# Optimization experiments

Hardware: AMD Instinct MI355X
Metric: run time of the kernel (lower is better)

## Reference

```python
import jax, jax.numpy as jnp
import numpy as np

B, S, E, H = 2, 2048, 512, 8
D = E // H  # head size = 64
LN_EPS = 1e-5


def setup_inputs() -> dict:
    key = jax.random.key(0)
    ks = jax.random.split(key, 8)
    s_in = 1.0 / np.sqrt(E)
    return {
        "x": jax.random.normal(ks[0], (B, S, E), jnp.float32),
        # per-head projection weights, stored [H, E, D] so q = x @ Wq[h]
        "Wq": jax.random.normal(ks[1], (H, E, D), jnp.float32) * s_in,
        "Wk": jax.random.normal(ks[2], (H, E, D), jnp.float32) * s_in,
        "Wv": jax.random.normal(ks[3], (H, E, D), jnp.float32) * s_in,
        "Wp": jax.random.normal(ks[4], (E, E), jnp.float32) * s_in,
        "bp": jnp.zeros((E,), jnp.float32),
        "gamma": jnp.ones((E,), jnp.float32),
        "beta": jnp.zeros((E,), jnp.float32),
        # causal mask buffer: masked_fill where mask == 0
        "mask": jnp.tril(jnp.ones((S, S), jnp.int32)),
    }


def reference(x, Wq, Wk, Wv, Wp, bp, gamma, beta, mask):
    # batched per-head projections (equivalent to the H small Linears)
    q = jnp.einsum("bse,hed->bhsd", x, Wq)
    k = jnp.einsum("bse,hed->bhsd", x, Wk)
    v = jnp.einsum("bse,hed->bhsd", x, Wv)
    # NOTE: original has NO 1/sqrt(d) scaling
    att_log = jnp.einsum("bhsd,bhtd->bhst", q, k)
    att_log = jnp.where(mask == 0, -jnp.inf, att_log)
    att = jax.nn.softmax(att_log, axis=-1)
    o = jnp.einsum("bhst,bhtd->bhsd", att, v)  # [B,H,S,D]
    # torch.cat((val, values)) prepends each head -> final order head H-1 .. 0
    o = o[:, ::-1]
    vals = o.transpose(0, 2, 1, 3).reshape(B, S, E)
    out = vals @ Wp.T + bp + x
    mu = jnp.mean(out, axis=-1, keepdims=True)
    var = jnp.var(out, axis=-1, keepdims=True)
    return (out - mu) * jax.lax.rsqrt(var + LN_EPS) * gamma + beta
```

## Files before the change

kernel.cpp:

```cpp
#include <hip/hip_runtime.h>

constexpr int Bn = 2;
constexpr int Sn = 2048;
constexpr int En = 512;
constexpr int Hn = 8;
constexpr int Dn = 64;
constexpr int Mn = Bn * Sn;

typedef short bf8 __attribute__((ext_vector_type(8)));
typedef float f32x4 __attribute__((ext_vector_type(4)));

constexpr size_t XY = (size_t)Mn * En;
constexpr size_t WT = (size_t)3 * En * En;
constexpr size_t WP = (size_t)En * En;
constexpr size_t PL = (size_t)Bn * Hn * Sn * Dn;
constexpr size_t MLP = (size_t)512 * 64 * 2;
constexpr size_t OPP = (size_t)512 * 64 * 64;

__device__ __forceinline__ unsigned short f2bf(float f) {
    unsigned int u = __float_as_uint(f);
    unsigned int r = 0x7FFFu + ((u >> 16) & 1u);
    return (unsigned short)((u + r) >> 16);
}
__device__ __forceinline__ float bf2f(unsigned short u) {
    return __uint_as_float(((unsigned int)u) << 16);
}
__device__ __forceinline__ void split2(float f, unsigned short& hi, unsigned short& lo) {
    hi = f2bf(f);
    lo = f2bf(f - bf2f(hi));
}

__device__ __forceinline__ void g2l16(const unsigned short* g, unsigned short* l) {
    typedef __attribute__((address_space(1))) const unsigned int gu32;
    typedef __attribute__((address_space(3))) unsigned int lu32;
    __builtin_amdgcn_global_load_lds((gu32*)(unsigned long long)g,
                                     (lu32*)(unsigned int)(unsigned long long)l,
                                     16, 0, 0);
}

__global__ __launch_bounds__(256)
void prep(const float* __restrict__ x, const float* __restrict__ Wp,
          const float* __restrict__ Wq, const float* __restrict__ Wk,
          const float* __restrict__ Wv,
          unsigned short* __restrict__ xh, unsigned short* __restrict__ xl,
          unsigned short* __restrict__ Wph, unsigned short* __restrict__ Wpl,
          unsigned short* __restrict__ Wth, unsigned short* __restrict__ Wtl)
{
    __shared__ float t[64][65];
    const int bid = blockIdx.x;
    const int tid = threadIdx.x;

    if (bid < 1152) {
        const float* src = (bid < 1024) ? x : Wp;
        unsigned short* hp = (bid < 1024) ? xh : Wph;
        unsigned short* lp = (bid < 1024) ? xl : Wpl;
        const int blk = (bid < 1024) ? bid : (bid - 1024);
        const size_t base = ((size_t)blk * 256 + tid) * 8;
        float a[8];
        *(float4*)&a[0] = *(const float4*)(src + base);
        *(float4*)&a[4] = *(const float4*)(src + base + 4);
        unsigned short h[8], l[8];
        #pragma unroll
        for (int j = 0; j < 8; ++j) split2(a[j], h[j], l[j]);
        *(bf8*)(hp + base) = *(bf8*)&h[0];
        *(bf8*)(lp + base) = *(bf8*)&l[0];
        return;
    }

    const int idx = bid - 1152;
    const int ph = idx >> 3;
    const int proj = ph >> 3, h = ph & 7;
    const int e0 = (idx & 7) * 64;
    const float* W = (proj == 0) ? Wq : (proj == 1) ? Wk : Wv;
    const float* src = W + (size_t)h * En * Dn + (size_t)e0 * Dn;

    const int er = tid >> 2, cg = (tid & 3) * 16;
    #pragma unroll
    for (int c = 0; c < 4; ++c) {
        float4 v = *(const float4*)(src + (size_t)er * Dn + cg + 4 * c);
        t[er][cg + 4 * c + 0] = v.x;
        t[er][cg + 4 * c + 1] = v.y;
        t[er][cg + 4 * c + 2] = v.z;
        t[er][cg + 4 * c + 3] = v.w;
    }
    __syncthreads();

    const int d = tid >> 2, jg = (tid & 3) * 16;
    unsigned short h16[16], l16[16];
    #pragma unroll
    for (int j = 0; j < 16; ++j) split2(t[jg + j][d], h16[j], l16[j]);
    const size_t n = (size_t)proj * 512 + h * 64 + d;
    unsigned short* dh = Wth + n * En + e0 + jg;
    unsigned short* dl = Wtl + n * En + e0 + jg;
    *(bf8*)dh       = *(bf8*)&h16[0];
    *(bf8*)(dh + 8) = *(bf8*)&h16[8];
    *(bf8*)dl       = *(bf8*)&l16[0];
    *(bf8*)(dl + 8) = *(bf8*)&l16[8];
}

__global__ __launch_bounds__(256)
void qkv_gemm(const unsigned short* __restrict__ xh,
              const unsigned short* __restrict__ xl,
              const unsigned short* __restrict__ Wth,
              const unsigned short* __restrict__ Wtl,
              unsigned short* __restrict__ qh_g,
              unsigned short* __restrict__ ql_g,
              unsigned short* __restrict__ kh_g,
              unsigned short* __restrict__ kl_g,
              unsigned short* __restrict__ vT_g)
{
    __shared__ __align__(16) unsigned char smraw[49152];
    unsigned short* ldsAh = (unsigned short*)smraw;
    unsigned short* ldsAl = ldsAh + 8192;
    unsigned short* ldsBh = ldsAl + 8192;
    unsigned short* ldsBl = ldsBh + 4096;
    float (*Cf)[68] = (float(*)[68])(smraw);

    const int tid = threadIdx.x;
    const int m0 = blockIdx.x * 128;
    const int ny = blockIdx.y;
    const int proj = ny >> 3, h = ny & 7;

    const int wave = tid >> 6, lane = tid & 63;
    const int wm = (wave >> 1) * 64, wn = (wave & 1) * 32;
    const int lm = lane & 15, quad = lane >> 4;

    const int l4r = lane >> 2;
    const int l4c = (lane & 3) * 8;
    const unsigned short* gAh0 = xh + (size_t)(m0 + wave * 32 + l4r) * En + l4c;
    const unsigned short* gAh1 = gAh0 + (size_t)16 * En;
    const unsigned short* gAl0 = xl + (size_t)(m0 + wave * 32 + l4r) * En + l4c;
    const unsigned short* gAl1 = gAl0 + (size_t)16 * En;
    const unsigned short* gBh  = Wth + (size_t)(ny * 64 + wave * 16 + l4r) * En + l4c;
    const unsigned short* gBl  = Wtl + (size_t)(ny * 64 + wave * 16 + l4r) * En + l4c;
    const int offA = wave * 1024;
    const int offB = wave * 512;

    f32x4 acc[4][2];
    #pragma unroll
    for (int i = 0; i < 4; ++i)
        #pragma unroll
        for (int j = 0; j < 2; ++j) acc[i][j] = (f32x4){0.f, 0.f, 0.f, 0.f};

    g2l16(gAh0, ldsAh + offA);
    g2l16(gAh1, ldsAh + offA + 512);
    g2l16(gAl0, ldsAl + offA);
    g2l16(gAl1, ldsAl + offA + 512);
    g2l16(gBh,  ldsBh + offB);
    g2l16(gBl,  ldsBl + offB);

    int cur = 0;
    for (int k0 = 0; k0 < En; k0 += 32) {
        __syncthreads();
        const int nxt = cur ^ 1;
        if (k0 + 32 < En) {
            g2l16(gAh0 + k0 + 32, ldsAh + nxt * 4096 + offA);
            g2l16(gAh1 + k0 + 32, ldsAh + nxt * 4096 + offA + 512);
            g2l16(gAl0 + k0 + 32, ldsAl + nxt * 4096 + offA);
            g2l16(gAl1 + k0 + 32, ldsAl + nxt * 4096 + offA + 512);
            g2l16(gBh + k0 + 32,  ldsBh + nxt * 2048 + offB);
            g2l16(gBl + k0 + 32,  ldsBl + nxt * 2048 + offB);
        }

        const unsigned short* bAh = ldsAh + cur * 4096;
        const unsigned short* bAl = ldsAl + cur * 4096;
        const unsigned short* bBh = ldsBh + cur * 2048;
        const unsigned short* bBl = ldsBl + cur * 2048;
        bf8 a_h[4], a_l[4], b_h[2], b_l[2];
        #pragma unroll
        for (int mi = 0; mi < 4; ++mi) {
            a_h[mi] = *(const bf8*)(bAh + (wm + mi * 16 + lm) * 32 + quad * 8);
            a_l[mi] = *(const bf8*)(bAl + (wm + mi * 16 + lm) * 32 + quad * 8);
        }
        #pragma unroll
        for (int ni = 0; ni < 2; ++ni) {
            b_h[ni] = *(const bf8*)(bBh + (wn + ni * 16 + lm) * 32 + quad * 8);
            b_l[ni] = *(const bf8*)(bBl + (wn + ni * 16 + lm) * 32 + quad * 8);
        }
        #pragma unroll
        for (int mi = 0; mi < 4; ++mi)
            #pragma unroll
            for (int ni = 0; ni < 2; ++ni) {
                acc[mi][ni] = __builtin_amdgcn_mfma_f32_16x16x32_bf16(a_h[mi], b_h[ni], acc[mi][ni], 0, 0, 0);
                acc[mi][ni] = __builtin_amdgcn_mfma_f32_16x16x32_bf16(a_h[mi], b_l[ni], acc[mi][ni], 0, 0, 0);
                acc[mi][ni] = __builtin_amdgcn_mfma_f32_16x16x32_bf16(a_l[mi], b_h[ni], acc[mi][ni], 0, 0, 0);
            }
        cur = nxt;
    }
    __syncthreads();

    if (proj < 2) {
        unsigned short* hp = (proj == 0) ? qh_g : kh_g;
        unsigned short* lp = (proj == 0) ? ql_g : kl_g;
        #pragma unroll
        for (int p = 0; p < 2; ++p) {
            if ((wave >> 1) == p) {
                #pragma unroll
                for (int mi = 0; mi < 4; ++mi)
                    #pragma unroll
                    for (int ni = 0; ni < 2; ++ni)
                        #pragma unroll
                        for (int r = 0; r < 4; ++r)
                            Cf[mi * 16 + quad * 4 + r][wn + ni * 16 + lm] = acc[mi][ni][r];
            }
            __syncthreads();
            {
                const int lr = tid & 63;
                const int cg = (tid >> 6) * 16;
                const int m = m0 + p * 64 + lr;
                const int b = m >> 11, s = m & 2047;
                unsigned short hi[16], lo[16];
                #pragma unroll
                for (int j4 = 0; j4 < 4; ++j4) {
                    float4 v = *(const float4*)&Cf[lr][cg + 4 * j4];
                    split2(v.x, hi[4 * j4 + 0], lo[4 * j4 + 0]);
                    split2(v.y, hi[4 * j4 + 1], lo[4 * j4 + 1]);
                    split2(v.z, hi[4 * j4 + 2], lo[4 * j4 + 2]);
                    split2(v.w, hi[4 * j4 + 3], lo[4 * j4 + 3]);
                }
                const size_t base = (((size_t)(b * Hn + h) * Sn + s) * Dn) + cg;
                *(bf8*)(hp + base)     = *(bf8*)&hi[0];
                *(bf8*)(hp + base + 8) = *(bf8*)&hi[8];
                *(bf8*)(lp + base)     = *(bf8*)&lo[0];
                *(bf8*)(lp + base + 8) = *(bf8*)&lo[8];
            }
            __syncthreads();
        }
    } else {
        #pragma unroll
        for (int mi = 0; mi < 4; ++mi) {
            const int s0 = m0 + wm + mi * 16 + quad * 4;
            const int b = s0 >> 11, s = s0 & 2047;
            #pragma unroll
            for (int ni = 0; ni < 2; ++ni) {
                const int d = wn + ni * 16 + lm;
                ushort4 pk;
                pk.x = f2bf(acc[mi][ni][0]);
                pk.y = f2bf(acc[mi][ni][1]);
                pk.z = f2bf(acc[mi][ni][2]);
                pk.w = f2bf(acc[mi][ni][3]);
                *(ushort4*)(vT_g + ((size_t)(b * Hn + h) * Dn + d) * Sn + s) = pk;
            }
        }
    }
}

__global__ __launch_bounds__(512, 4)
void attn(const unsigned short* __restrict__ qh_g,
          const unsigned short* __restrict__ ql_g,
          const unsigned short* __restrict__ kh_g,
          const unsigned short* __restrict__ kl_g,
          const unsigned short* __restrict__ vT_g,
          unsigned short* __restrict__ Op,
          float* __restrict__ ml)
{
    extern __shared__ unsigned short sm[];
    unsigned short (*khs)[72] = (unsigned short(*)[72])(sm);
    unsigned short (*kls)[72] = (unsigned short(*)[72])(sm + 4608);
    unsigned short (*vTs)[72] = (unsigned short(*)[72])(sm + 9216);
    unsigned short (*pts)[72] = (unsigned short(*)[72])(sm + 13824);
    float* alf = (float*)(sm + 23040);

    const int bidx = blockIdx.x;
    const int xcd = bidx & 7;
    const int g = bidx >> 3;
    const int bh = xcd * 2 + (g & 1);
    const int p2 = g >> 1;
    const int qp = p2 & 15;
    const int sb = p2 >> 4;

    const int tid = threadIdx.x;
    const int wave = tid >> 6, lane = tid & 63;
    const int quad = lane >> 4, lq = lane & 15;
    const int wq = wave >> 2;
    const int w4 = wave & 3;

    const unsigned short* khb = kh_g + (size_t)bh * Sn * Dn;
    const unsigned short* klb = kl_g + (size_t)bh * Sn * Dn;
    const unsigned short* vTb = vT_g + (size_t)bh * Dn * Sn;

    const int srow = tid & 63;
    const int sdg  = tid >> 6;

    #pragma unroll 1
    for (int ph = 0; ph < 2; ++ph) {
        const int qt = ph ? (15 - qp) : qp;
        const int j  = ph ? (3 - sb) : sb;
        const int n  = 2 * qt + 2;
        const int its = (j * n) >> 2;
        const int ite = ((j + 1) * n) >> 2;
        const int qt64 = 2 * qt + wq;
        const int pslot = j * 512 + bh * 32 + qt64;
        const int dt = qt64;

        bf8 qfh[2], qfl[2];
        {
            const size_t qoff = ((size_t)bh * Sn + (size_t)qt * 128 + wave * 16 + lq) * Dn;
            #pragma unroll
            for (int c = 0; c < 2; ++c) {
                qfh[c] = *(const bf8*)(qh_g + qoff + c * 32 + quad * 8);
                qfl[c] = *(const bf8*)(ql_g + qoff + c * 32 + quad * 8);
            }
        }

        f32x4 accO[4];
        #pragma unroll
        for (int nj = 0; nj < 4; ++nj) accO[nj] = (f32x4){0.f, 0.f, 0.f, 0.f};
        float m = -1e30f, l = 0.f;

        bf8 pk0 = {0, 0, 0, 0, 0, 0, 0, 0};
        bf8 pl0 = {0, 0, 0, 0, 0, 0, 0, 0};
        bf8 pv0 = {0, 0, 0, 0, 0, 0, 0, 0};
        if (its < ite) {
            const int t0 = its * 64;
            pk0 = *(const bf8*)(khb + (size_t)(t0 + srow) * Dn + sdg * 8);
            pl0 = *(const bf8*)(klb + (size_t)(t0 + srow) * Dn + sdg * 8);
            pv0 = *(const bf8*)(vTb + (size_t)srow * Sn + t0 + sdg * 8);
        }

        for (int it = its; it < ite; ++it) {
            __syncthreads();
            *(bf8*)&khs[srow][sdg * 8] = pk0;
            *(bf8*)&kls[srow][sdg * 8] = pl0;
            *(bf8*)&vTs[srow][sdg * 8] = pv0;
            __syncthreads();

            if (it + 1 < ite) {
                const int t1 = (it + 1) * 64;
                pk0 = *(const bf8*)(khb + (size_t)(t1 + srow) * Dn + sdg * 8);
                pl0 = *(const bf8*)(klb + (size_t)(t1 + srow) * Dn + sdg * 8);
                pv0 = *(const bf8*)(vTb + (size_t)srow * Sn + t1 + sdg * 8);
            }

            if (it > dt) continue;

            f32x4 accS[4];
            #pragma unroll
            for (int mi = 0; mi < 4; ++mi) accS[mi] = (f32x4){0.f, 0.f, 0.f, 0.f};
            __builtin_amdgcn_s_setprio(1);
            #pragma unroll
            for (int mi = 0; mi < 4; ++mi) {
                #pragma unroll
                for (int c = 0; c < 2; ++c) {
                    bf8 ah = *(const bf8*)&khs[mi * 16 + lq][c * 32 + quad * 8];
                    bf8 al = *(const bf8*)&kls[mi * 16 + lq][c * 32 + quad * 8];
                    accS[mi] = __builtin_amdgcn_mfma_f32_16x16x32_bf16(ah, qfh[c], accS[mi], 0, 0, 0);
                    accS[mi] = __builtin_amdgcn_mfma_f32_16x16x32_bf16(ah, qfl[c], accS[mi], 0, 0, 0);
                    accS[mi] = __builtin_amdgcn_mfma_f32_16x16x32_bf16(al, qfh[c], accS[mi], 0, 0, 0);
                }
            }
            __builtin_amdgcn_s_setprio(0);

            if (it == dt) {
                const int qrel = w4 * 16 + lq;
                #pragma unroll
                for (int mi = 0; mi < 4; ++mi)
                    #pragma unroll
                    for (int r = 0; r < 4; ++r)
                        if (mi * 16 + quad * 4 + r > qrel) accS[mi][r] = -INFINITY;
            }

            float mt;
            {
                float t0 = fmaxf(fmaxf(accS[0][0], accS[0][1]), fmaxf(accS[0][2], accS[0][3]));
                float t1 = fmaxf(fmaxf(accS[1][0], accS[1][1]), fmaxf(accS[1][2], accS[1][3]));
                float t2 = fmaxf(fmaxf(accS[2][0], accS[2][1]), fmaxf(accS[2][2], accS[2][3]));
                float t3 = fmaxf(fmaxf(accS[3][0], accS[3][1]), fmaxf(accS[3][2], accS[3][3]));
                mt = fmaxf(fmaxf(t0, t1), fmaxf(t2, t3));
            }
            mt = fmaxf(mt, __shfl_xor(mt, 16));
            mt = fmaxf(mt, __shfl_xor(mt, 32));

            const bool defer = __all(mt <= m + 12.f);
            float mref, alpha = 1.f;
            if (defer) {
                mref = m;
            } else {
                mref = fmaxf(m, mt);
                alpha = __expf(m - mref);
            }

            float ls = 0.f;
            #pragma unroll
            for (int mi = 0; mi < 4; ++mi)
                #pragma unroll
                for (int r = 0; r < 4; ++r) {
                    const float p = __expf(accS[mi][r] - mref);
                    accS[mi][r] = p;
                    ls += p;
                }
            ls += __shfl_xor(ls, 16);
            ls += __shfl_xor(ls, 32);
            if (defer) {
                l += ls;
            } else {
                l = l * alpha + ls;
                m = mref;
            }

            #pragma unroll
            for (int mi = 0; mi < 4; ++mi) {
                ushort4 pk;
                pk.x = f2bf(accS[mi][0]);
                pk.y = f2bf(accS[mi][1]);
                pk.z = f2bf(accS[mi][2]);
                pk.w = f2bf(accS[mi][3]);
                *(ushort4*)&pts[wave * 16 + lq][mi * 16 + quad * 4] = pk;
            }

            if (!defer) {
                if (quad == 0) alf[wave * 16 + lq] = alpha;
                float4 al4 = *(const float4*)&alf[wave * 16 + quad * 4];
                #pragma unroll
                for (int nj = 0; nj < 4; ++nj) {
                    accO[nj][0] *= al4.x;
                    accO[nj][1] *= al4.y;
                    accO[nj][2] *= al4.z;
                    accO[nj][3] *= al4.w;
                }
            }

            __builtin_amdgcn_s_setprio(1);
            #pragma unroll
            for (int c = 0; c < 2; ++c) {
                bf8 pf = *(const bf8*)&pts[wave * 16 + lq][c * 32 + quad * 8];
                #pragma unroll
                for (int nj = 0; nj < 4; ++nj) {
                    bf8 vf = *(const bf8*)&vTs[nj * 16 + lq][c * 32 + quad * 8];
                    accO[nj] = __builtin_amdgcn_mfma_f32_16x16x32_bf16(pf, vf, accO[nj], 0, 0, 0);
                }
            }
            __builtin_amdgcn_s_setprio(0);
        }

        if (quad == 0) {
            const size_t mi_ = ((size_t)pslot * 64 + w4 * 16 + lq) * 2;
            ml[mi_]     = m;
            ml[mi_ + 1] = l;
        }
        #pragma unroll
        for (int r = 0; r < 4; ++r) {
            const int q = w4 * 16 + quad * 4 + r;
            unsigned short* dst = Op + ((size_t)pslot * 64 + q) * 64;
            #pragma unroll
            for (int nj = 0; nj < 4; ++nj)
                dst[nj * 16 + lq] = f2bf(accO[nj][r]);
        }
    }
}

__global__ __launch_bounds__(256)
void out_gemm(const unsigned short* __restrict__ Op,
              const float* __restrict__ ml,
              const unsigned short* __restrict__ Wph,
              const unsigned short* __restrict__ Wpl,
              const float* __restrict__ bp,
              const float* __restrict__ x,
              float* __restrict__ outp,
              float* __restrict__ outp2)
{
    __shared__ unsigned short Ah[64][40], Al[64][40];
    __shared__ __align__(16) unsigned short Bh[128][32], Bl[128][32];

    const int tid = threadIdx.x;
    const int m0 = blockIdx.x * 64;
    const int n0 = blockIdx.y * 128;
    const int kz = blockIdx.z;
    const int kbeg = kz * 256, kend = kbeg + 256;

    const int wave = tid >> 6, lane = tid & 63;
    const int wm = (wave >> 1) * 32, wn = (wave & 1) * 64;
    const int lm = lane & 15, quad = lane >> 4;

    const int am = tid >> 2;
    const int aks = (tid & 3) * 8;
    const int m_row = m0 + am;
    const int b_row = m_row >> 11, s_row = m_row & 2047;
    const int qt = s_row >> 6, qq = s_row & 63;

    float c0[4], c1[4], c2[4], c3[4];
    #pragma unroll
    for (int hl = 0; hl < 4; ++hl) {
        const int h = hl + (kz ? 0 : 4);
        const size_t base0 = (((size_t)(b_row * 8 + h) * 32 + qt) * 64 + qq) * 2;
        float mi_[4], li_[4];
        #pragma unroll
        for (int i = 0; i < 4; ++i) {
            mi_[i] = ml[base0 + i * MLP];
            li_[i] = ml[base0 + i * MLP + 1];
        }
        const float mn = fmaxf(fmaxf(mi_[0], mi_[1]), fmaxf(mi_[2], mi_[3]));
        const float a0 = __expf(mi_[0] - mn), a1 = __expf(mi_[1] - mn);
        const float a2 = __expf(mi_[2] - mn), a3 = __expf(mi_[3] - mn);
        const float inv = 1.f / (a0 * li_[0] + a1 * li_[1] + a2 * li_[2] + a3 * li_[3]);
        c0[hl] = a0 * inv;
        c1[hl] = a1 * inv;
        c2[hl] = a2 * inv;
        c3[hl] = a3 * inv;
    }

    const int l4r = lane >> 2;
    const int l4c = (lane & 3) * 8;
    const unsigned short* gB0h = Wph + (size_t)(n0 + wave * 32 + l4r) * En + l4c;
    const unsigned short* gB1h = gB0h + (size_t)16 * En;
    const unsigned short* gB0l = Wpl + (size_t)(n0 + wave * 32 + l4r) * En + l4c;
    const unsigned short* gB1l = gB0l + (size_t)16 * En;
    unsigned short* dB0h = &Bh[0][0] + wave * 1024;
    unsigned short* dB1h = dB0h + 512;
    unsigned short* dB0l = &Bl[0][0] + wave * 1024;
    unsigned short* dB1l = dB0l + 512;

    f32x4 acc[2][4];
    #pragma unroll
    for (int i = 0; i < 2; ++i)
        #pragma unroll
        for (int j = 0; j < 4; ++j) acc[i][j] = (f32x4){0.f, 0.f, 0.f, 0.f};

    bf8 po0, po1, po2, po3;
    {
        const int e0 = kbeg + aks;
        const int hh = 7 - (e0 >> 6);
        const int dd = e0 & 63;
        const size_t p0 = (((size_t)((b_row * 8 + hh) * 32 + qt)) * 64 + qq) * 64 + dd;
        po0 = *(const bf8*)(Op + p0);
        po1 = *(const bf8*)(Op + p0 + OPP);
        po2 = *(const bf8*)(Op + p0 + 2 * OPP);
        po3 = *(const bf8*)(Op + p0 + 3 * OPP);
    }

    for (int k0 = kbeg; k0 < kend; k0 += 32) {
        g2l16(gB0h + k0, dB0h);
        g2l16(gB1h + k0, dB1h);
        g2l16(gB0l + k0, dB0l);
        g2l16(gB1l + k0, dB1l);
        {
            const int hidx = (7 - ((k0 + aks) >> 6)) & 3;
            const float w0 = c0[hidx], w1 = c1[hidx];
            const float w2 = c2[hidx], w3 = c3[hidx];
            unsigned short hi[8], lo[8];
            #pragma unroll
            for (int j = 0; j < 8; ++j) {
                const float v = w0 * bf2f((unsigned short)po0[j]) +
                                w1 * bf2f((unsigned short)po1[j]) +
                                w2 * bf2f((unsigned short)po2[j]) +
                                w3 * bf2f((unsigned short)po3[j]);
                split2(v, hi[j], lo[j]);
            }
            *(bf8*)&Ah[am][aks] = *(bf8*)&hi[0];
            *(bf8*)&Al[am][aks] = *(bf8*)&lo[0];
        }
        __syncthreads();

        if (k0 + 32 < kend) {
            const int e0 = k0 + 32 + aks;
            const int hh = 7 - (e0 >> 6);
            const int dd = e0 & 63;
            const size_t p0 = (((size_t)((b_row * 8 + hh) * 32 + qt)) * 64 + qq) * 64 + dd;
            po0 = *(const bf8*)(Op + p0);
            po1 = *(const bf8*)(Op + p0 + OPP);
            po2 = *(const bf8*)(Op + p0 + 2 * OPP);
            po3 = *(const bf8*)(Op + p0 + 3 * OPP);
        }

        bf8 a_h[2], a_l[2], b_h[4], b_l[4];
        #pragma unroll
        for (int mi = 0; mi < 2; ++mi) {
            a_h[mi] = *(const bf8*)&Ah[wm + mi * 16 + lm][quad * 8];
            a_l[mi] = *(const bf8*)&Al[wm + mi * 16 + lm][quad * 8];
        }
        #pragma unroll
        for (int ni = 0; ni < 4; ++ni) {
            b_h[ni] = *(const bf8*)&Bh[wn + ni * 16 + lm][quad * 8];
            b_l[ni] = *(const bf8*)&Bl[wn + ni * 16 + lm][quad * 8];
        }
        #pragma unroll
        for (int mi = 0; mi < 2; ++mi)
            #pragma unroll
            for (int ni = 0; ni < 4; ++ni) {
                acc[mi][ni] = __builtin_amdgcn_mfma_f32_16x16x32_bf16(a_h[mi], b_h[ni], acc[mi][ni], 0, 0, 0);
                acc[mi][ni] = __builtin_amdgcn_mfma_f32_16x16x32_bf16(a_h[mi], b_l[ni], acc[mi][ni], 0, 0, 0);
                acc[mi][ni] = __builtin_amdgcn_mfma_f32_16x16x32_bf16(a_l[mi], b_h[ni], acc[mi][ni], 0, 0, 0);
            }
        __syncthreads();
    }

    float* dst = kz ? outp2 : outp;
    #pragma unroll
    for (int mi = 0; mi < 2; ++mi) {
        #pragma unroll
        for (int r = 0; r < 4; ++r) {
            const int m = m0 + wm + mi * 16 + quad * 4 + r;
            #pragma unroll
            for (int ni = 0; ni < 4; ++ni) {
                const int n = n0 + wn + ni * 16 + lm;
                const size_t idx = (size_t)m * En + n;
                const float extra = kz ? 0.f : (bp[n] + x[idx]);
                dst[idx] = acc[mi][ni][r] + extra;
            }
        }
    }
}

__global__ __launch_bounds__(256)
void ln_kernel(const float* __restrict__ outp,
               const float* __restrict__ outp2,
               const float* __restrict__ gamma,
               const float* __restrict__ beta,
               float* __restrict__ y)
{
    const int row = blockIdx.x * 4 + (threadIdx.x >> 6);
    const int lane = threadIdx.x & 63;
    const size_t off = (size_t)row * En + lane * 8;

    float a[8], b2[8];
    *(float4*)&a[0] = *(const float4*)(outp + off);
    *(float4*)&a[4] = *(const float4*)(outp + off + 4);
    *(float4*)&b2[0] = *(const float4*)(outp2 + off);
    *(float4*)&b2[4] = *(const float4*)(outp2 + off + 4);
    #pragma unroll
    for (int j = 0; j < 8; ++j) a[j] += b2[j];

    float sum = 0.f, sq = 0.f;
    #pragma unroll
    for (int j = 0; j < 8; ++j) { sum += a[j]; sq += a[j] * a[j]; }
    #pragma unroll
    for (int off_ = 1; off_ < 64; off_ <<= 1) {
        sum += __shfl_xor(sum, off_);
        sq  += __shfl_xor(sq, off_);
    }
    const float mu = sum * (1.f / 512.f);
    const float var = sq * (1.f / 512.f) - mu * mu;
    const float rs = rsqrtf(var + 1e-5f);

    const float* g = gamma + lane * 8;
    const float* be = beta + lane * 8;
    float o[8];
    #pragma unroll
    for (int j = 0; j < 8; ++j)
        o[j] = (a[j] - mu) * rs * g[j] + be[j];
    float* yr = y + off;
    *(float4*)(yr)     = *(float4*)&o[0];
    *(float4*)(yr + 4) = *(float4*)&o[4];
}

extern "C" void kernel_launch(void* const* d_in, const int* in_sizes, int n_in,
                              void* d_out, int out_size, void* d_ws, size_t ws_size,
                              hipStream_t stream)
{
    const float* x     = (const float*)d_in[0];
    const float* Wq    = (const float*)d_in[1];
    const float* Wk    = (const float*)d_in[2];
    const float* Wv    = (const float*)d_in[3];
    const float* Wp    = (const float*)d_in[4];
    const float* bp    = (const float*)d_in[5];
    const float* gamma = (const float*)d_in[6];
    const float* beta  = (const float*)d_in[7];

    float* ws   = (float*)d_ws;
    float* ml   = ws;
    float* outp = ws + XY;
    unsigned short* bfb = (unsigned short*)(ws + 2 * XY);
    unsigned short* xh  = bfb;
    unsigned short* xl  = bfb + XY;
    unsigned short* Wth = bfb + 2 * XY;
    unsigned short* Wtl = Wth + WT;
    unsigned short* Wph = Wtl + WT;
    unsigned short* Wpl = Wph + WP;
    unsigned short* qh  = Wpl + WP;
    unsigned short* ql  = qh + PL;
    unsigned short* kh  = ql + PL;
    unsigned short* kl  = kh + PL;
    unsigned short* vT  = kl + PL;
    unsigned short* Op  = vT + PL;
    float* outp2 = (float*)qh;

    const int attn_lds = 46592;
    hipFuncSetAttribute((const void*)attn,
                        hipFuncAttributeMaxDynamicSharedMemorySize, attn_lds);

    prep<<<dim3(1344), 256, 0, stream>>>(x, Wp, Wq, Wk, Wv,
                                         xh, xl, Wph, Wpl, Wth, Wtl);
    qkv_gemm<<<dim3(Mn / 128, 24), 256, 0, stream>>>(xh, xl, Wth, Wtl,
                                                     qh, ql, kh, kl, vT);
    attn<<<dim3(512), 512, attn_lds, stream>>>(qh, ql, kh, kl, vT, Op, ml);
    out_gemm<<<dim3(Mn / 64, En / 128, 2), 256, 0, stream>>>(Op, ml, Wph, Wpl,
                                                             bp, x, outp, outp2);
    ln_kernel<<<dim3(Mn / 4), 256, 0, stream>>>(outp, outp2, gamma, beta,
                                                (float*)d_out);
}
```

Before: 170.7 us.

## Double-buffer attention K/V LDS tiles and remap GEMM grids per XCD

The attention kernel now keeps two LDS buffers for the K-hi, K-lo and V^T tiles, which removes one of the two barriers per KV iteration. The global prefetch is pushed two tiles ahead. The QKV and output GEMMs switch to 1-D grids whose block index is remapped so that neighbouring M tiles land on the same XCD, aiming for better L2 reuse. The cost is a larger attention LDS footprint (about 74KB instead of 46KB), which may lower occupancy per CU.

```diff
diff --git a/kernel.cpp b/kernel.cpp
--- a/kernel.cpp
+++ b/kernel.cpp
@@ -117,8 +117,11 @@
     float (*Cf)[68] = (float(*)[68])(smraw);
 
     const int tid = threadIdx.x;
-    const int m0 = blockIdx.x * 128;
-    const int ny = blockIdx.y;
+    const int bid = blockIdx.x;
+    const int xcd = bid & 7;
+    const int loc = bid >> 3;
+    const int m0 = (xcd * 4 + (loc & 3)) * 128;
+    const int ny = loc >> 2;
     const int proj = ny >> 3, h = ny & 7;
 
     const int wave = tid >> 6, lane = tid & 63;
@@ -255,11 +258,11 @@
           float* __restrict__ ml)
 {
     extern __shared__ unsigned short sm[];
-    unsigned short (*khs)[72] = (unsigned short(*)[72])(sm);
-    unsigned short (*kls)[72] = (unsigned short(*)[72])(sm + 4608);
-    unsigned short (*vTs)[72] = (unsigned short(*)[72])(sm + 9216);
-    unsigned short (*pts)[72] = (unsigned short(*)[72])(sm + 13824);
-    float* alf = (float*)(sm + 23040);
+    #define KHS(p) (sm + (p) * 4608)
+    #define KLS(p) (sm + 9216 + (p) * 4608)
+    #define VTS(p) (sm + 18432 + (p) * 4608)
+    unsigned short (*pts)[72] = (unsigned short(*)[72])(sm + 27648);
+    float* alf = (float*)(sm + 36864);
 
     const int bidx = blockIdx.x;
     const int xcd = bidx & 7;
@@ -281,6 +284,7 @@
 
     const int srow = tid & 63;
     const int sdg  = tid >> 6;
+    const int soff = srow * 72 + sdg * 8;
 
     #pragma unroll 1
     for (int ph = 0; ph < 2; ++ph) {
@@ -308,31 +312,43 @@
         for (int nj = 0; nj < 4; ++nj) accO[nj] = (f32x4){0.f, 0.f, 0.f, 0.f};
         float m = -1e30f, l = 0.f;
 
-        bf8 pk0 = {0, 0, 0, 0, 0, 0, 0, 0};
-        bf8 pl0 = {0, 0, 0, 0, 0, 0, 0, 0};
-        bf8 pv0 = {0, 0, 0, 0, 0, 0, 0, 0};
+        bf8 rk = {0, 0, 0, 0, 0, 0, 0, 0};
+        bf8 rl = {0, 0, 0, 0, 0, 0, 0, 0};
+        bf8 rv = {0, 0, 0, 0, 0, 0, 0, 0};
         if (its < ite) {
             const int t0 = its * 64;
-            pk0 = *(const bf8*)(khb + (size_t)(t0 + srow) * Dn + sdg * 8);
-            pl0 = *(const bf8*)(klb + (size_t)(t0 + srow) * Dn + sdg * 8);
-            pv0 = *(const bf8*)(vTb + (size_t)srow * Sn + t0 + sdg * 8);
+            rk = *(const bf8*)(khb + (size_t)(t0 + srow) * Dn + sdg * 8);
+            rl = *(const bf8*)(klb + (size_t)(t0 + srow) * Dn + sdg * 8);
+            rv = *(const bf8*)(vTb + (size_t)srow * Sn + t0 + sdg * 8);
+            __syncthreads();
+            *(bf8*)(KHS(its & 1) + soff) = rk;
+            *(bf8*)(KLS(its & 1) + soff) = rl;
+            *(bf8*)(VTS(its & 1) + soff) = rv;
+            if (its + 1 < ite) {
+                const int t1 = (its + 1) * 64;
+                rk = *(const bf8*)(khb + (size_t)(t1 + srow) * Dn + sdg * 8);
+                rl = *(const bf8*)(klb + (size_t)(t1 + srow) * Dn + sdg * 8);
+                rv = *(const bf8*)(vTb + (size_t)srow * Sn + t1 + sdg * 8);
+            }
         }
 
         for (int it = its; it < ite; ++it) {
             __syncthreads();
-            *(bf8*)&khs[srow][sdg * 8] = pk0;
-            *(bf8*)&kls[srow][sdg * 8] = pl0;
-            *(bf8*)&vTs[srow][sdg * 8] = pv0;
-            __syncthreads();
-
             if (it + 1 < ite) {
-                const int t1 = (it + 1) * 64;
-                pk0 = *(const bf8*)(khb + (size_t)(t1 + srow) * Dn + sdg * 8);
-                pl0 = *(const bf8*)(klb + (size_t)(t1 + srow) * Dn + sdg * 8);
-                pv0 = *(const bf8*)(vTb + (size_t)srow * Sn + t1 + sdg * 8);
+                const int p1 = (it + 1) & 1;
+                *(bf8*)(KHS(p1) + soff) = rk;
+                *(bf8*)(KLS(p1) + soff) = rl;
+                *(bf8*)(VTS(p1) + soff) = rv;
+                if (it + 2 < ite) {
+                    const int t2 = (it + 2) * 64;
+                    rk = *(const bf8*)(khb + (size_t)(t2 + srow) * Dn + sdg * 8);
+                    rl = *(const bf8*)(klb + (size_t)(t2 + srow) * Dn + sdg * 8);
+                    rv = *(const bf8*)(vTb + (size_t)srow * Sn + t2 + sdg * 8);
+                }
             }
 
             if (it > dt) continue;
+            const int p = it & 1;
 
             f32x4 accS[4];
             #pragma unroll
@@ -342,8 +358,8 @@
             for (int mi = 0; mi < 4; ++mi) {
                 #pragma unroll
                 for (int c = 0; c < 2; ++c) {
-                    bf8 ah = *(const bf8*)&khs[mi * 16 + lq][c * 32 + quad * 8];
-                    bf8 al = *(const bf8*)&kls[mi * 16 + lq][c * 32 + quad * 8];
+                    bf8 ah = *(const bf8*)(KHS(p) + (mi * 16 + lq) * 72 + c * 32 + quad * 8);
+                    bf8 al = *(const bf8*)(KLS(p) + (mi * 16 + lq) * 72 + c * 32 + quad * 8);
                     accS[mi] = __builtin_amdgcn_mfma_f32_16x16x32_bf16(ah, qfh[c], accS[mi], 0, 0, 0);
                     accS[mi] = __builtin_amdgcn_mfma_f32_16x16x32_bf16(ah, qfl[c], accS[mi], 0, 0, 0);
                     accS[mi] = __builtin_amdgcn_mfma_f32_16x16x32_bf16(al, qfh[c], accS[mi], 0, 0, 0);
@@ -385,9 +401,9 @@
             for (int mi = 0; mi < 4; ++mi)
                 #pragma unroll
                 for (int r = 0; r < 4; ++r) {
-                    const float p = __expf(accS[mi][r] - mref);
-                    accS[mi][r] = p;
-                    ls += p;
+                    const float p_ = __expf(accS[mi][r] - mref);
+                    accS[mi][r] = p_;
+                    ls += p_;
                 }
             ls += __shfl_xor(ls, 16);
             ls += __shfl_xor(ls, 32);
@@ -426,7 +442,7 @@
                 bf8 pf = *(const bf8*)&pts[wave * 16 + lq][c * 32 + quad * 8];
                 #pragma unroll
                 for (int nj = 0; nj < 4; ++nj) {
-                    bf8 vf = *(const bf8*)&vTs[nj * 16 + lq][c * 32 + quad * 8];
+                    bf8 vf = *(const bf8*)(VTS(p) + (nj * 16 + lq) * 72 + c * 32 + quad * 8);
                     accO[nj] = __builtin_amdgcn_mfma_f32_16x16x32_bf16(pf, vf, accO[nj], 0, 0, 0);
                 }
             }
@@ -447,6 +463,9 @@
                 dst[nj * 16 + lq] = f2bf(accO[nj][r]);
         }
     }
+    #undef KHS
+    #undef KLS
+    #undef VTS
 }
 
 __global__ __launch_bounds__(256)
@@ -463,9 +482,13 @@
     __shared__ __align__(16) unsigned short Bh[128][32], Bl[128][32];
 
     const int tid = threadIdx.x;
-    const int m0 = blockIdx.x * 64;
-    const int n0 = blockIdx.y * 128;
-    const int kz = blockIdx.z;
+    const int bid = blockIdx.x;
+    const int xcd = bid & 7;
+    const int loc = bid >> 3;
+    const int m0 = (xcd * 8 + (loc & 7)) * 64;
+    const int rest = loc >> 3;
+    const int n0 = (rest & 3) * 128;
+    const int kz = rest >> 2;
     const int kbeg = kz * 256, kend = kbeg + 256;
 
     const int wave = tid >> 6, lane = tid & 63;
@@ -674,17 +697,17 @@
     unsigned short* Op  = vT + PL;
     float* outp2 = (float*)qh;
 
-    const int attn_lds = 46592;
+    const int attn_lds = 74240;
     hipFuncSetAttribute((const void*)attn,
                         hipFuncAttributeMaxDynamicSharedMemorySize, attn_lds);
 
     prep<<<dim3(1344), 256, 0, stream>>>(x, Wp, Wq, Wk, Wv,
                                          xh, xl, Wph, Wpl, Wth, Wtl);
-    qkv_gemm<<<dim3(Mn / 128, 24), 256, 0, stream>>>(xh, xl, Wth, Wtl,
-                                                     qh, ql, kh, kl, vT);
+    qkv_gemm<<<dim3(768), 256, 0, stream>>>(xh, xl, Wth, Wtl,
+                                            qh, ql, kh, kl, vT);
     attn<<<dim3(512), 512, attn_lds, stream>>>(qh, ql, kh, kl, vT, Op, ml);
-    out_gemm<<<dim3(Mn / 64, En / 128, 2), 256, 0, stream>>>(Op, ml, Wph, Wpl,
-                                                             bp, x, outp, outp2);
+    out_gemm<<<dim3(512), 256, 0, stream>>>(Op, ml, Wph, Wpl,
+                                            bp, x, outp, outp2);
     ln_kernel<<<dim3(Mn / 4), 256, 0, stream>>>(outp, outp2, gamma, beta,
                                                 (float*)d_out);
 }
```

Result: no change. 172.4 us (+1.0%).

## Stage attention output through LDS for coalesced stores; double-buffer Wp tiles

Applied to the files above, without the earlier changes.

The attention kernel now writes its per-tile bf16 output into shared memory and then stores it to global memory with 16-byte vector writes per thread. Previously each lane wrote scattered 2-byte elements. The output GEMM double-buffers the Wp hi/lo shared tiles, issuing the global-to-LDS copy for the next k-step before computing the current one, so load latency can overlap the MFMAs. The cost is two extra barriers in the attention epilogue and twice the B-tile shared memory, which may lower occupancy.

```diff
diff --git a/kernel.cpp b/kernel.cpp
--- a/kernel.cpp
+++ b/kernel.cpp
@@ -438,13 +438,23 @@
             ml[mi_]     = m;
             ml[mi_ + 1] = l;
         }
+
+        __syncthreads();
         #pragma unroll
         for (int r = 0; r < 4; ++r) {
-            const int q = w4 * 16 + quad * 4 + r;
-            unsigned short* dst = Op + ((size_t)pslot * 64 + q) * 64;
+            const int lrow = wq * 64 + w4 * 16 + quad * 4 + r;
             #pragma unroll
             for (int nj = 0; nj < 4; ++nj)
-                dst[nj * 16 + lq] = f2bf(accO[nj][r]);
+                pts[lrow][nj * 16 + lq] = f2bf(accO[nj][r]);
+        }
+        __syncthreads();
+        {
+            const int row = tid >> 2;
+            const int cg  = (tid & 3) * 16;
+            const int ps  = j * 512 + bh * 32 + 2 * qt + (row >> 6);
+            unsigned short* dst = Op + ((size_t)ps * 64 + (row & 63)) * 64 + cg;
+            *(bf8*)(dst)     = *(const bf8*)&pts[row][cg];
+            *(bf8*)(dst + 8) = *(const bf8*)&pts[row][cg + 8];
         }
     }
 }
@@ -460,7 +470,7 @@
               float* __restrict__ outp2)
 {
     __shared__ unsigned short Ah[64][40], Al[64][40];
-    __shared__ __align__(16) unsigned short Bh[128][32], Bl[128][32];
+    __shared__ __align__(16) unsigned short Bh[2][128][32], Bl[2][128][32];
 
     const int tid = threadIdx.x;
     const int m0 = blockIdx.x * 64;
@@ -505,10 +515,7 @@
     const unsigned short* gB1h = gB0h + (size_t)16 * En;
     const unsigned short* gB0l = Wpl + (size_t)(n0 + wave * 32 + l4r) * En + l4c;
     const unsigned short* gB1l = gB0l + (size_t)16 * En;
-    unsigned short* dB0h = &Bh[0][0] + wave * 1024;
-    unsigned short* dB1h = dB0h + 512;
-    unsigned short* dB0l = &Bl[0][0] + wave * 1024;
-    unsigned short* dB1l = dB0l + 512;
+    const int offB = wave * 1024;
 
     f32x4 acc[2][4];
     #pragma unroll
@@ -528,11 +535,13 @@
         po3 = *(const bf8*)(Op + p0 + 3 * OPP);
     }
 
+    g2l16(gB0h + kbeg, &Bh[0][0][0] + offB);
+    g2l16(gB1h + kbeg, &Bh[0][0][0] + offB + 512);
+    g2l16(gB0l + kbeg, &Bl[0][0][0] + offB);
+    g2l16(gB1l + kbeg, &Bl[0][0][0] + offB + 512);
+
+    int cur = 0;
     for (int k0 = kbeg; k0 < kend; k0 += 32) {
-        g2l16(gB0h + k0, dB0h);
-        g2l16(gB1h + k0, dB1h);
-        g2l16(gB0l + k0, dB0l);
-        g2l16(gB1l + k0, dB1l);
         {
             const int hidx = (7 - ((k0 + aks) >> 6)) & 3;
             const float w0 = c0[hidx], w1 = c1[hidx];
@@ -551,7 +560,12 @@
         }
         __syncthreads();
 
+        const int nxt = cur ^ 1;
         if (k0 + 32 < kend) {
+            g2l16(gB0h + k0 + 32, &Bh[nxt][0][0] + offB);
+            g2l16(gB1h + k0 + 32, &Bh[nxt][0][0] + offB + 512);
+            g2l16(gB0l + k0 + 32, &Bl[nxt][0][0] + offB);
+            g2l16(gB1l + k0 + 32, &Bl[nxt][0][0] + offB + 512);
             const int e0 = k0 + 32 + aks;
             const int hh = 7 - (e0 >> 6);
             const int dd = e0 & 63;
@@ -570,8 +584,8 @@
         }
         #pragma unroll
         for (int ni = 0; ni < 4; ++ni) {
-            b_h[ni] = *(const bf8*)&Bh[wn + ni * 16 + lm][quad * 8];
-            b_l[ni] = *(const bf8*)&Bl[wn + ni * 16 + lm][quad * 8];
+            b_h[ni] = *(const bf8*)&Bh[cur][wn + ni * 16 + lm][quad * 8];
+            b_l[ni] = *(const bf8*)&Bl[cur][wn + ni * 16 + lm][quad * 8];
         }
         #pragma unroll
         for (int mi = 0; mi < 2; ++mi)
@@ -582,6 +596,7 @@
                 acc[mi][ni] = __builtin_amdgcn_mfma_f32_16x16x32_bf16(a_l[mi], b_h[ni], acc[mi][ni], 0, 0, 0);
             }
         __syncthreads();
+        cur = nxt;
     }
 
     float* dst = kz ? outp2 : outp;
```

Result: no change. 171.3 us (+0.3%).
